# Performance work log

Measured on AMD Instinct MI355X. Metric: run time of the kernel, lower is better.

Reference implementation:

```python
import jax, jax.numpy as jnp
import numpy as np

N_NODES = 100000
N_EDGES = 1600000
N_GRAPHS = 64
IN_CH = 128
HIDDEN = 128
OUT_CH = 2


def gcn_conv(x, row, col, W, b, num_nodes):
    # PyG GCNConv: add self-loops, symmetric deg^{-1/2} normalization,
    # linear transform, scatter-add aggregation, then bias.
    loop = jnp.arange(num_nodes, dtype=row.dtype)
    r = jnp.concatenate([row, loop])  # source nodes
    c = jnp.concatenate([col, loop])  # target nodes
    deg = jax.ops.segment_sum(jnp.ones_like(c, dtype=x.dtype), c, num_segments=num_nodes)
    dinv = jnp.where(deg > 0, jax.lax.rsqrt(deg), 0.0)
    norm = dinv[r] * dinv[c]  # [E+N]
    h = x @ W  # [N, F_out]
    msg = norm[:, None] * h[r]  # gather [E+N, F_out]
    agg = jax.ops.segment_sum(msg, c, num_segments=num_nodes)  # scatter-add
    return agg + b


def setup_inputs() -> dict:
    key = jax.random.key(0)
    ks = jax.random.split(key, 8)
    x = jax.random.normal(ks[0], (N_NODES, IN_CH), dtype=jnp.float32)
    edge_index = jax.random.randint(ks[1], (2, N_EDGES), 0, N_NODES, dtype=jnp.int32)
    batch = jnp.sort(jax.random.randint(ks[2], (N_NODES,), 0, N_GRAPHS, dtype=jnp.int32))
    s1 = 1.0 / np.sqrt(IN_CH)
    s2 = 1.0 / np.sqrt(HIDDEN)
    W1 = jax.random.normal(ks[3], (IN_CH, HIDDEN), dtype=jnp.float32) * s1
    b1 = jnp.zeros((HIDDEN,), dtype=jnp.float32)
    W2 = jax.random.normal(ks[4], (HIDDEN, HIDDEN), dtype=jnp.float32) * s2
    b2 = jnp.zeros((HIDDEN,), dtype=jnp.float32)
    Wlin = jax.random.normal(ks[5], (HIDDEN, OUT_CH), dtype=jnp.float32) * s2
    blin = jnp.zeros((OUT_CH,), dtype=jnp.float32)
    return {"x": x, "edge_index": edge_index, "batch": batch,
            "W1": W1, "b1": b1, "W2": W2, "b2": b2, "Wlin": Wlin, "blin": blin}


def reference(x, edge_index, batch, W1, b1, W2, b2, Wlin, blin):
    row, col = edge_index[0], edge_index[1]
    h = jax.nn.relu(gcn_conv(x, row, col, W1, b1, N_NODES))
    h = jax.nn.relu(gcn_conv(h, row, col, W2, b2, N_NODES))
    # global_mean_pool over graph ids
    sums = jax.ops.segment_sum(h, batch, num_segments=N_GRAPHS)  # [G, H]
    cnts = jax.ops.segment_sum(jnp.ones((h.shape[0],), dtype=h.dtype), batch, num_segments=N_GRAPHS)
    pooled = sums / jnp.maximum(cnts, 1.0)[:, None]
    return pooled @ Wlin + blin  # [G, OUT_CH]
```

## Files before the change

kernel.cpp:

```cpp
#include <hip/hip_runtime.h>
#include <hip/hip_bf16.h>
#include <hip/hip_fp16.h>

#define N_NODES  100000
#define N_EDGES  1600000
#define N_GRAPHS 64

#define NB       256
#define BSZ      391
#define NE4      (N_EDGES/4)
#define NBLK     391

typedef __attribute__((ext_vector_type(4))) float    f32x4;
typedef __attribute__((ext_vector_type(8))) _Float16 f16x8;

__global__ __launch_bounds__(256) void zero_kernel(float* __restrict__ pooled,
                                                   float* __restrict__ gcnt) {
    int i = blockIdx.x * 256 + threadIdx.x;
    if (i < N_GRAPHS * 128) pooled[i] = 0.f;
    if (i < N_GRAPHS) gcnt[i] = 0.f;
}

__global__ __launch_bounds__(256) void sortcount_kernel(const int4* __restrict__ col4,
                                                        int* __restrict__ blockcnt) {
    __shared__ int hist[NB];
    int t = threadIdx.x, blk = blockIdx.x;
    hist[t] = 0;
    __syncthreads();
#pragma unroll
    for (int j = 0; j < 4; ++j) {
        int i = blk * 1024 + j * 256 + t;
        if (i < NE4) {
            int4 c = col4[i];
            atomicAdd(&hist[c.x / BSZ], 1);
            atomicAdd(&hist[c.y / BSZ], 1);
            atomicAdd(&hist[c.z / BSZ], 1);
            atomicAdd(&hist[c.w / BSZ], 1);
        }
    }
    __syncthreads();
    blockcnt[blk * NB + t] = hist[t];
}

__global__ __launch_bounds__(256) void sortscan_kernel(int* __restrict__ blockcnt,
                                                       int* __restrict__ buckettotal) {
    int b = blockIdx.x, t = threadIdx.x;
    __shared__ int sc[256];
    int e0 = 2 * t, e1 = 2 * t + 1;
    int v0 = (e0 < NBLK) ? blockcnt[e0 * NB + b] : 0;
    int v1 = (e1 < NBLK) ? blockcnt[e1 * NB + b] : 0;
    int ps = v0 + v1;
    sc[t] = ps;
    __syncthreads();
    for (int d = 1; d < 256; d <<= 1) {
        int x = (t >= d) ? sc[t - d] : 0;
        __syncthreads();
        sc[t] += x;
        __syncthreads();
    }
    int ex = sc[t] - ps;
    if (e0 < NBLK) blockcnt[e0 * NB + b] = ex;
    if (e1 < NBLK) blockcnt[e1 * NB + b] = ex + v0;
    if (t == 255) buckettotal[b] = sc[255];
}

__global__ __launch_bounds__(256) void sortbase_kernel(const int* __restrict__ buckettotal,
                                                       int* __restrict__ bucket_base,
                                                       int* __restrict__ off) {
    __shared__ int sc[256];
    int t = threadIdx.x;
    int v = buckettotal[t];
    sc[t] = v;
    __syncthreads();
    for (int d = 1; d < 256; d <<= 1) {
        int x = (t >= d) ? sc[t - d] : 0;
        __syncthreads();
        sc[t] += x;
        __syncthreads();
    }
    bucket_base[t] = sc[t] - v;
    if (t == 255) {
        bucket_base[256] = sc[255];
        off[N_NODES] = N_EDGES;
    }
}

__global__ __launch_bounds__(256) void sortscatter_kernel(const int4* __restrict__ row4,
                                                          const int4* __restrict__ col4,
                                                          const int* __restrict__ blockpre,
                                                          const int* __restrict__ bucket_base,
                                                          int2* __restrict__ pairs) {
    __shared__ int cur[NB];
    int t = threadIdx.x, blk = blockIdx.x;
    cur[t] = bucket_base[t] + blockpre[blk * NB + t];
    __syncthreads();
#pragma unroll
    for (int j = 0; j < 4; ++j) {
        int i = blk * 1024 + j * 256 + t;
        if (i < NE4) {
            int4 r = row4[i];
            int4 c = col4[i];
            int p0 = atomicAdd(&cur[c.x / BSZ], 1); pairs[p0] = make_int2(r.x, c.x);
            int p1 = atomicAdd(&cur[c.y / BSZ], 1); pairs[p1] = make_int2(r.y, c.y);
            int p2 = atomicAdd(&cur[c.z / BSZ], 1); pairs[p2] = make_int2(r.z, c.z);
            int p3 = atomicAdd(&cur[c.w / BSZ], 1); pairs[p3] = make_int2(r.w, c.w);
        }
    }
}

__global__ __launch_bounds__(256) void sortlocal_kernel(const int2* __restrict__ pairs,
                                                        const int* __restrict__ bucket_base,
                                                        const int* __restrict__ buckettotal,
                                                        int* __restrict__ sortr,
                                                        int* __restrict__ off,
                                                        float* __restrict__ dinv) {
    int b = blockIdx.x, t = threadIdx.x;
    int base = bucket_base[b];
    int cnt  = buckettotal[b];
    int c0   = b * BSZ;
    int nc   = N_NODES - c0; if (nc > BSZ) nc = BSZ;

    __shared__ int hist[BSZ];
    __shared__ int sc[256];
    for (int i = t; i < nc; i += 256) hist[i] = 0;
    __syncthreads();
    for (int i = t; i < cnt; i += 256) {
        int2 pc = pairs[base + i];
        atomicAdd(&hist[pc.y - c0], 1);
    }
    __syncthreads();
    int e0 = 2 * t, e1 = 2 * t + 1;
    int h0 = (e0 < nc) ? hist[e0] : 0;
    int h1 = (e1 < nc) ? hist[e1] : 0;
    int ps = h0 + h1;
    sc[t] = ps;
    __syncthreads();
    for (int d = 1; d < 256; d <<= 1) {
        int x = (t >= d) ? sc[t - d] : 0;
        __syncthreads();
        sc[t] += x;
        __syncthreads();
    }
    int ex = sc[t] - ps;
    if (e0 < nc) { off[c0 + e0] = base + ex;      dinv[c0 + e0] = rsqrtf((float)h0 + 1.f); }
    if (e1 < nc) { off[c0 + e1] = base + ex + h0; dinv[c0 + e1] = rsqrtf((float)h1 + 1.f); }
    __syncthreads();
    if (e0 < nc) hist[e0] = base + ex;
    if (e1 < nc) hist[e1] = base + ex + h0;
    __syncthreads();
    for (int i = t; i < cnt; i += 256) {
        int2 pc = pairs[base + i];
        int pos = atomicAdd(&hist[pc.y - c0], 1);
        sortr[pos] = pc.x;
    }
}

__global__ __launch_bounds__(256) void wpack_kernel(const float* __restrict__ W1,
                                                    const float* __restrict__ W2,
                                                    _Float16* __restrict__ Wp1,
                                                    _Float16* __restrict__ Wp2) {
    int tid = blockIdx.x * 256 + threadIdx.x;
    const float* W = (tid < 2048) ? W1 : W2;
    _Float16*   Wp = (tid < 2048) ? Wp1 : Wp2;
    int t = tid & 2047;
    int f = t >> 6, lane = t & 63;
    int j = f >> 2, s = f & 3;
    int kb = s * 32 + (lane >> 4) * 8;
    int c  = j * 16 + (lane & 15);
#pragma unroll
    for (int i = 0; i < 8; ++i)
        Wp[(size_t)t * 8 + i] = (_Float16)W[(kb + i) * 128 + c];
}

template<int FP16IN>
__global__ __launch_bounds__(256) void gemm_mfma_kernel(const void* __restrict__ Xv,
                                                        const _Float16* __restrict__ Wp,
                                                        const float* __restrict__ dinv,
                                                        _Float16* __restrict__ out) {
    __shared__ _Float16 Wl[16384];
    {
        const float4* src = (const float4*)Wp;
        float4* dst = (float4*)Wl;
        for (int i = threadIdx.x; i < 2048; i += 256) dst[i] = src[i];
    }
    __syncthreads();

    int wv = threadIdx.x >> 6, lane = threadIdx.x & 63;
    int tile = blockIdx.x * 4 + wv;
    if (tile >= N_NODES / 16) return;
    int n0 = tile * 16;
    int m = lane & 15, b = lane >> 4;

    f16x8 a[4];
    if (FP16IN) {
        const _Float16* X = (const _Float16*)Xv;
        const _Float16* base = X + (size_t)(n0 + m) * 128 + b * 8;
#pragma unroll
        for (int s = 0; s < 4; ++s) a[s] = *(const f16x8*)(base + s * 32);
    } else {
        const float* X = (const float*)Xv;
        const float* base = X + (size_t)(n0 + m) * 128 + b * 8;
#pragma unroll
        for (int s = 0; s < 4; ++s) {
            float4 u = *(const float4*)(base + s * 32);
            float4 v = *(const float4*)(base + s * 32 + 4);
            f16x8 tt;
            tt[0] = (_Float16)u.x; tt[1] = (_Float16)u.y;
            tt[2] = (_Float16)u.z; tt[3] = (_Float16)u.w;
            tt[4] = (_Float16)v.x; tt[5] = (_Float16)v.y;
            tt[6] = (_Float16)v.z; tt[7] = (_Float16)v.w;
            a[s] = tt;
        }
    }

    f32x4 acc[8];
#pragma unroll
    for (int j = 0; j < 8; ++j) acc[j] = (f32x4){0.f, 0.f, 0.f, 0.f};

#pragma unroll
    for (int j = 0; j < 8; ++j) {
#pragma unroll
        for (int s = 0; s < 4; ++s) {
            f16x8 bf = *(const f16x8*)&Wl[(j * 4 + s) * 512 + lane * 8];
            acc[j] = __builtin_amdgcn_mfma_f32_16x16x32_f16(a[s], bf, acc[j], 0, 0, 0);
        }
    }

    float dv0 = dinv[n0 + b * 4 + 0];
    float dv1 = dinv[n0 + b * 4 + 1];
    float dv2 = dinv[n0 + b * 4 + 2];
    float dv3 = dinv[n0 + b * 4 + 3];
#pragma unroll
    for (int j = 0; j < 8; ++j) {
        _Float16* o = out + (size_t)(n0 + b * 4) * 128 + j * 16 + m;
        o[0 * 128] = (_Float16)(acc[j][0] * dv0);
        o[1 * 128] = (_Float16)(acc[j][1] * dv1);
        o[2 * 128] = (_Float16)(acc[j][2] * dv2);
        o[3 * 128] = (_Float16)(acc[j][3] * dv3);
    }
}

__global__ __launch_bounds__(256) void agg_kernel(const __half* __restrict__ hs,
                                                  const int* __restrict__ sortr,
                                                  const int* __restrict__ off,
                                                  const float* __restrict__ dinv,
                                                  const float* __restrict__ bias,
                                                  __half* __restrict__ out) {
    int wid = (blockIdx.x * 256 + threadIdx.x) >> 6;
    int lane = threadIdx.x & 63;
    if (wid >= N_NODES) return;
    const int c = wid;
    const int e0 = off[c], e1 = off[c + 1];
    const long chb = 2 * lane;

    float2 s = __half22float2(*(const __half2*)&hs[(long)c * 128 + chb]);
    float a0x = s.x, a0y = s.y;
    float a1x = 0.f, a1y = 0.f, a2x = 0.f, a2y = 0.f, a3x = 0.f, a3y = 0.f;

    int e = e0;
    for (; e + 4 <= e1; e += 4) {
        int r0 = sortr[e + 0], r1 = sortr[e + 1];
        int r2 = sortr[e + 2], r3 = sortr[e + 3];
        float2 v0 = __half22float2(*(const __half2*)&hs[(long)r0 * 128 + chb]);
        float2 v1 = __half22float2(*(const __half2*)&hs[(long)r1 * 128 + chb]);
        float2 v2 = __half22float2(*(const __half2*)&hs[(long)r2 * 128 + chb]);
        float2 v3 = __half22float2(*(const __half2*)&hs[(long)r3 * 128 + chb]);
        a0x += v0.x; a0y += v0.y;
        a1x += v1.x; a1y += v1.y;
        a2x += v2.x; a2y += v2.y;
        a3x += v3.x; a3y += v3.y;
    }
    for (; e < e1; ++e) {
        int r0 = sortr[e];
        float2 v0 = __half22float2(*(const __half2*)&hs[(long)r0 * 128 + chb]);
        a0x += v0.x; a0y += v0.y;
    }
    float ax = (a0x + a1x) + (a2x + a3x);
    float ay = (a0y + a1y) + (a2y + a3y);

    float dv = dinv[c];
    float2 bb = *(const float2*)&bias[chb];
    float rx = fmaxf(fmaf(ax, dv, bb.x), 0.f);
    float ry = fmaxf(fmaf(ay, dv, bb.y), 0.f);
    *(__half2*)&out[(long)c * 128 + chb] = __floats2half2_rn(rx, ry);
}

__global__ __launch_bounds__(256) void pool_kernel(const __half* __restrict__ h,
                                                   const int* __restrict__ batch,
                                                   float* __restrict__ pooled,
                                                   float* __restrict__ gcnt) {
    int wid = (blockIdx.x * 256 + threadIdx.x) >> 6;
    int lane = threadIdx.x & 63;
    long n0 = (long)wid * 32;
    if (n0 >= N_NODES) return;
    long n1 = n0 + 32;
    if (n1 > N_NODES) n1 = N_NODES;
    const long chb = 2 * lane;

    int g = batch[n0];
    float ax = 0.f, ay = 0.f;
    int run = 0;
    for (long n = n0; n < n1; ++n) {
        int gn = batch[n];
        if (gn != g) {
            atomicAdd(&pooled[g * 128 + chb], ax);
            atomicAdd(&pooled[g * 128 + chb + 1], ay);
            if (lane == 0) atomicAdd(&gcnt[g], (float)run);
            g = gn; ax = 0.f; ay = 0.f; run = 0;
        }
        float2 v = __half22float2(*(const __half2*)&h[n * 128 + chb]);
        ax += v.x; ay += v.y; run++;
    }
    atomicAdd(&pooled[g * 128 + chb], ax);
    atomicAdd(&pooled[g * 128 + chb + 1], ay);
    if (lane == 0) atomicAdd(&gcnt[g], (float)run);
}

__global__ void final_kernel(const float* __restrict__ pooled,
                             const float* __restrict__ gcnt,
                             const float* __restrict__ Wlin,
                             const float* __restrict__ blin,
                             float* __restrict__ out) {
    int t = threadIdx.x;
    if (t >= N_GRAPHS * 2) return;
    int g = t >> 1, o = t & 1;
    float c = gcnt[g];
    if (c < 1.f) c = 1.f;
    float s = 0.f;
    for (int k = 0; k < 128; ++k)
        s += (pooled[g * 128 + k] / c) * Wlin[k * 2 + o];
    out[g * 2 + o] = s + blin[o];
}

extern "C" void kernel_launch(void* const* d_in, const int* in_sizes, int n_in,
                              void* d_out, int out_size, void* d_ws, size_t ws_size,
                              hipStream_t stream) {
    const float* x     = (const float*)d_in[0];
    const int*   row   = (const int*)d_in[1];
    const int*   col   = row + N_EDGES;
    const int*   batch = (const int*)d_in[2];
    const float* W1    = (const float*)d_in[3];
    const float* b1    = (const float*)d_in[4];
    const float* W2    = (const float*)d_in[5];
    const float* b2    = (const float*)d_in[6];
    const float* Wlin  = (const float*)d_in[7];
    const float* blin  = (const float*)d_in[8];
    float* out = (float*)d_out;

    char* w = (char*)d_ws;
    size_t p = 0;
    auto alloc = [&](size_t bytes) -> void* {
        void* r = w + p;
        p += (bytes + 511) & ~(size_t)511;
        return r;
    };
    int*      off         = (int*)alloc((size_t)(N_NODES + 1) * 4);
    float*    dinv        = (float*)alloc((size_t)N_NODES * 4);
    int*      sortr       = (int*)alloc((size_t)N_EDGES * 4);
    int2*     pairs       = (int2*)alloc((size_t)N_EDGES * 8);
    int*      blockcnt    = (int*)alloc((size_t)NBLK * NB * 4);
    int*      buckettotal = (int*)alloc((size_t)NB * 4);
    int*      bucket_base = (int*)alloc((size_t)(NB + 1) * 4);
    _Float16* Wp1         = (_Float16*)alloc((size_t)128 * 128 * 2);
    _Float16* Wp2         = (_Float16*)alloc((size_t)128 * 128 * 2);
    __half*   hs          = (__half*)alloc((size_t)N_NODES * 128 * 2);
    __half*   hbuf        = (__half*)alloc((size_t)N_NODES * 128 * 2);
    float*    pooled      = (float*)alloc((size_t)N_GRAPHS * 128 * 4);
    float*    gcnt        = (float*)alloc((size_t)N_GRAPHS * 4);
    (void)ws_size; (void)in_sizes; (void)n_in; (void)out_size;

    zero_kernel<<<(N_GRAPHS * 128 + 255) / 256, 256, 0, stream>>>(pooled, gcnt);

    sortcount_kernel<<<NBLK, 256, 0, stream>>>((const int4*)col, blockcnt);
    sortscan_kernel<<<NB, 256, 0, stream>>>(blockcnt, buckettotal);
    sortbase_kernel<<<1, 256, 0, stream>>>(buckettotal, bucket_base, off);
    sortscatter_kernel<<<NBLK, 256, 0, stream>>>((const int4*)row, (const int4*)col,
                                                 blockcnt, bucket_base, pairs);
    sortlocal_kernel<<<NB, 256, 0, stream>>>(pairs, bucket_base, buckettotal,
                                             sortr, off, dinv);

    wpack_kernel<<<16, 256, 0, stream>>>(W1, W2, Wp1, Wp2);

    gemm_mfma_kernel<0><<<(N_NODES / 16 + 3) / 4, 256, 0, stream>>>(x, Wp1, dinv, (_Float16*)hs);
    agg_kernel<<<(N_NODES * 64 + 255) / 256, 256, 0, stream>>>(hs, sortr, off, dinv, b1, hbuf);
    gemm_mfma_kernel<1><<<(N_NODES / 16 + 3) / 4, 256, 0, stream>>>(hbuf, Wp2, dinv, (_Float16*)hs);
    agg_kernel<<<(N_NODES * 64 + 255) / 256, 256, 0, stream>>>(hs, sortr, off, dinv, b2, hbuf);

    pool_kernel<<<(((N_NODES + 31) / 32) * 64 + 255) / 256, 256, 0, stream>>>(hbuf, batch, pooled, gcnt);
    final_kernel<<<1, 128, 0, stream>>>(pooled, gcnt, Wlin, blin, out);
}
```

Measured before the change: 356.1 us.

## Fuse aggregation with next GEMM and pooling, pack sort pairs into one int

The first GCN aggregation is fused with the second layer's MFMA GEMM through a shared-memory row buffer. The second aggregation is fused with global mean pooling using per-block reductions before the atomics. Sort pairs are packed into a single 32-bit word (local column in the high bits, row in the low 17 bits), halving the pairs traffic. Zeroing is folded into the weight-pack kernel. Together these remove two intermediate N×128 buffer round trips and three launches. In exchange, the fused GEMM reads W from global memory instead of LDS, and each block gathers only 16 rows, which may lower latency hiding.

```diff
diff --git a/kernel.cpp b/kernel.cpp
--- a/kernel.cpp
+++ b/kernel.cpp
@@ -10,16 +10,10 @@
 #define BSZ      391
 #define NE4      (N_EDGES/4)
 #define NBLK     391
+#define ROWMASK  0x1FFFF
 
 typedef __attribute__((ext_vector_type(4))) float    f32x4;
 typedef __attribute__((ext_vector_type(8))) _Float16 f16x8;
-
-__global__ __launch_bounds__(256) void zero_kernel(float* __restrict__ pooled,
-                                                   float* __restrict__ gcnt) {
-    int i = blockIdx.x * 256 + threadIdx.x;
-    if (i < N_GRAPHS * 128) pooled[i] = 0.f;
-    if (i < N_GRAPHS) gcnt[i] = 0.f;
-}
 
 __global__ __launch_bounds__(256) void sortcount_kernel(const int4* __restrict__ col4,
                                                         int* __restrict__ blockcnt) {
@@ -89,7 +83,7 @@
                                                           const int4* __restrict__ col4,
                                                           const int* __restrict__ blockpre,
                                                           const int* __restrict__ bucket_base,
-                                                          int2* __restrict__ pairs) {
+                                                          int* __restrict__ pairs) {
     __shared__ int cur[NB];
     int t = threadIdx.x, blk = blockIdx.x;
     cur[t] = bucket_base[t] + blockpre[blk * NB + t];
@@ -100,15 +94,16 @@
         if (i < NE4) {
             int4 r = row4[i];
             int4 c = col4[i];
-            int p0 = atomicAdd(&cur[c.x / BSZ], 1); pairs[p0] = make_int2(r.x, c.x);
-            int p1 = atomicAdd(&cur[c.y / BSZ], 1); pairs[p1] = make_int2(r.y, c.y);
-            int p2 = atomicAdd(&cur[c.z / BSZ], 1); pairs[p2] = make_int2(r.z, c.z);
-            int p3 = atomicAdd(&cur[c.w / BSZ], 1); pairs[p3] = make_int2(r.w, c.w);
-        }
-    }
-}
-
-__global__ __launch_bounds__(256) void sortlocal_kernel(const int2* __restrict__ pairs,
+            int b0 = c.x / BSZ, b1 = c.y / BSZ, b2 = c.z / BSZ, b3 = c.w / BSZ;
+            int p0 = atomicAdd(&cur[b0], 1); pairs[p0] = ((c.x - b0 * BSZ) << 17) | r.x;
+            int p1 = atomicAdd(&cur[b1], 1); pairs[p1] = ((c.y - b1 * BSZ) << 17) | r.y;
+            int p2 = atomicAdd(&cur[b2], 1); pairs[p2] = ((c.z - b2 * BSZ) << 17) | r.z;
+            int p3 = atomicAdd(&cur[b3], 1); pairs[p3] = ((c.w - b3 * BSZ) << 17) | r.w;
+        }
+    }
+}
+
+__global__ __launch_bounds__(256) void sortlocal_kernel(const int* __restrict__ pairs,
                                                         const int* __restrict__ bucket_base,
                                                         const int* __restrict__ buckettotal,
                                                         int* __restrict__ sortr,
@@ -125,8 +120,8 @@
     for (int i = t; i < nc; i += 256) hist[i] = 0;
     __syncthreads();
     for (int i = t; i < cnt; i += 256) {
-        int2 pc = pairs[base + i];
-        atomicAdd(&hist[pc.y - c0], 1);
+        int pc = pairs[base + i];
+        atomicAdd(&hist[pc >> 17], 1);
     }
     __syncthreads();
     int e0 = 2 * t, e1 = 2 * t + 1;
@@ -149,17 +144,23 @@
     if (e1 < nc) hist[e1] = base + ex + h0;
     __syncthreads();
     for (int i = t; i < cnt; i += 256) {
-        int2 pc = pairs[base + i];
-        int pos = atomicAdd(&hist[pc.y - c0], 1);
-        sortr[pos] = pc.x;
-    }
-}
-
-__global__ __launch_bounds__(256) void wpack_kernel(const float* __restrict__ W1,
-                                                    const float* __restrict__ W2,
-                                                    _Float16* __restrict__ Wp1,
-                                                    _Float16* __restrict__ Wp2) {
+        int pc = pairs[base + i];
+        int pos = atomicAdd(&hist[pc >> 17], 1);
+        sortr[pos] = pc & ROWMASK;
+    }
+}
+
+__global__ __launch_bounds__(256) void wpack_zero_kernel(const float* __restrict__ W1,
+                                                         const float* __restrict__ W2,
+                                                         _Float16* __restrict__ Wp1,
+                                                         _Float16* __restrict__ Wp2,
+                                                         float* __restrict__ pooled,
+                                                         float* __restrict__ gcnt) {
     int tid = blockIdx.x * 256 + threadIdx.x;
+    for (int i = tid; i < N_GRAPHS * 128 + N_GRAPHS; i += 4096) {
+        if (i < N_GRAPHS * 128) pooled[i] = 0.f;
+        else gcnt[i - N_GRAPHS * 128] = 0.f;
+    }
     const float* W = (tid < 2048) ? W1 : W2;
     _Float16*   Wp = (tid < 2048) ? Wp1 : Wp2;
     int t = tid & 2047;
@@ -172,8 +173,7 @@
         Wp[(size_t)t * 8 + i] = (_Float16)W[(kb + i) * 128 + c];
 }
 
-template<int FP16IN>
-__global__ __launch_bounds__(256) void gemm_mfma_kernel(const void* __restrict__ Xv,
+__global__ __launch_bounds__(256) void gemm_mfma_kernel(const float* __restrict__ X,
                                                         const _Float16* __restrict__ Wp,
                                                         const float* __restrict__ dinv,
                                                         _Float16* __restrict__ out) {
@@ -192,39 +192,29 @@
     int m = lane & 15, b = lane >> 4;
 
     f16x8 a[4];
-    if (FP16IN) {
-        const _Float16* X = (const _Float16*)Xv;
-        const _Float16* base = X + (size_t)(n0 + m) * 128 + b * 8;
-#pragma unroll
-        for (int s = 0; s < 4; ++s) a[s] = *(const f16x8*)(base + s * 32);
-    } else {
-        const float* X = (const float*)Xv;
-        const float* base = X + (size_t)(n0 + m) * 128 + b * 8;
-#pragma unroll
-        for (int s = 0; s < 4; ++s) {
-            float4 u = *(const float4*)(base + s * 32);
-            float4 v = *(const float4*)(base + s * 32 + 4);
-            f16x8 tt;
-            tt[0] = (_Float16)u.x; tt[1] = (_Float16)u.y;
-            tt[2] = (_Float16)u.z; tt[3] = (_Float16)u.w;
-            tt[4] = (_Float16)v.x; tt[5] = (_Float16)v.y;
-            tt[6] = (_Float16)v.z; tt[7] = (_Float16)v.w;
-            a[s] = tt;
-        }
+    const float* base = X + (size_t)(n0 + m) * 128 + b * 8;
+#pragma unroll
+    for (int s = 0; s < 4; ++s) {
+        float4 u = *(const float4*)(base + s * 32);
+        float4 v = *(const float4*)(base + s * 32 + 4);
+        f16x8 tt;
+        tt[0] = (_Float16)u.x; tt[1] = (_Float16)u.y;
+        tt[2] = (_Float16)u.z; tt[3] = (_Float16)u.w;
+        tt[4] = (_Float16)v.x; tt[5] = (_Float16)v.y;
+        tt[6] = (_Float16)v.z; tt[7] = (_Float16)v.w;
+        a[s] = tt;
     }
 
     f32x4 acc[8];
 #pragma unroll
     for (int j = 0; j < 8; ++j) acc[j] = (f32x4){0.f, 0.f, 0.f, 0.f};
-
-#pragma unroll
-    for (int j = 0; j < 8; ++j) {
+#pragma unroll
+    for (int j = 0; j < 8; ++j)
 #pragma unroll
         for (int s = 0; s < 4; ++s) {
             f16x8 bf = *(const f16x8*)&Wl[(j * 4 + s) * 512 + lane * 8];
             acc[j] = __builtin_amdgcn_mfma_f32_16x16x32_f16(a[s], bf, acc[j], 0, 0, 0);
         }
-    }
 
     float dv0 = dinv[n0 + b * 4 + 0];
     float dv1 = dinv[n0 + b * 4 + 1];
@@ -240,23 +230,12 @@
     }
 }
 
-__global__ __launch_bounds__(256) void agg_kernel(const __half* __restrict__ hs,
-                                                  const int* __restrict__ sortr,
-                                                  const int* __restrict__ off,
-                                                  const float* __restrict__ dinv,
-                                                  const float* __restrict__ bias,
-                                                  __half* __restrict__ out) {
-    int wid = (blockIdx.x * 256 + threadIdx.x) >> 6;
-    int lane = threadIdx.x & 63;
-    if (wid >= N_NODES) return;
-    const int c = wid;
-    const int e0 = off[c], e1 = off[c + 1];
-    const long chb = 2 * lane;
-
+__device__ __forceinline__ float2 gather_row(const __half* __restrict__ hs,
+                                             const int* __restrict__ sortr,
+                                             int c, int e0, int e1, long chb) {
     float2 s = __half22float2(*(const __half2*)&hs[(long)c * 128 + chb]);
     float a0x = s.x, a0y = s.y;
     float a1x = 0.f, a1y = 0.f, a2x = 0.f, a2y = 0.f, a3x = 0.f, a3y = 0.f;
-
     int e = e0;
     for (; e + 4 <= e1; e += 4) {
         int r0 = sortr[e + 0], r1 = sortr[e + 1];
@@ -275,45 +254,151 @@
         float2 v0 = __half22float2(*(const __half2*)&hs[(long)r0 * 128 + chb]);
         a0x += v0.x; a0y += v0.y;
     }
-    float ax = (a0x + a1x) + (a2x + a3x);
-    float ay = (a0y + a1y) + (a2y + a3y);
-
-    float dv = dinv[c];
+    float2 r;
+    r.x = (a0x + a1x) + (a2x + a3x);
+    r.y = (a0y + a1y) + (a2y + a3y);
+    return r;
+}
+
+__global__ __launch_bounds__(256) void agg_gemm_kernel(const __half* __restrict__ hs,
+                                                       const int* __restrict__ sortr,
+                                                       const int* __restrict__ off,
+                                                       const float* __restrict__ dinv,
+                                                       const float* __restrict__ bias,
+                                                       const _Float16* __restrict__ Wp,
+                                                       _Float16* __restrict__ out) {
+    __shared__ float rowbuf[16 * 132];
+    int t = threadIdx.x;
+    int wv = t >> 6, lane = t & 63;
+    int c0 = blockIdx.x * 16;
+    const long chb = 2 * (long)lane;
     float2 bb = *(const float2*)&bias[chb];
-    float rx = fmaxf(fmaf(ax, dv, bb.x), 0.f);
-    float ry = fmaxf(fmaf(ay, dv, bb.y), 0.f);
-    *(__half2*)&out[(long)c * 128 + chb] = __floats2half2_rn(rx, ry);
-}
-
-__global__ __launch_bounds__(256) void pool_kernel(const __half* __restrict__ h,
-                                                   const int* __restrict__ batch,
-                                                   float* __restrict__ pooled,
-                                                   float* __restrict__ gcnt) {
-    int wid = (blockIdx.x * 256 + threadIdx.x) >> 6;
-    int lane = threadIdx.x & 63;
-    long n0 = (long)wid * 32;
-    if (n0 >= N_NODES) return;
-    long n1 = n0 + 32;
-    if (n1 > N_NODES) n1 = N_NODES;
-    const long chb = 2 * lane;
-
-    int g = batch[n0];
-    float ax = 0.f, ay = 0.f;
-    int run = 0;
-    for (long n = n0; n < n1; ++n) {
-        int gn = batch[n];
-        if (gn != g) {
-            atomicAdd(&pooled[g * 128 + chb], ax);
-            atomicAdd(&pooled[g * 128 + chb + 1], ay);
-            if (lane == 0) atomicAdd(&gcnt[g], (float)run);
-            g = gn; ax = 0.f; ay = 0.f; run = 0;
-        }
-        float2 v = __half22float2(*(const __half2*)&h[n * 128 + chb]);
-        ax += v.x; ay += v.y; run++;
-    }
-    atomicAdd(&pooled[g * 128 + chb], ax);
-    atomicAdd(&pooled[g * 128 + chb + 1], ay);
-    if (lane == 0) atomicAdd(&gcnt[g], (float)run);
+
+#pragma unroll
+    for (int i = 0; i < 4; ++i) {
+        int c = c0 + wv * 4 + i;
+        float2 g = gather_row(hs, sortr, c, off[c], off[c + 1], chb);
+        float dv = dinv[c];
+        float rx = fmaxf(fmaf(g.x, dv, bb.x), 0.f);
+        float ry = fmaxf(fmaf(g.y, dv, bb.y), 0.f);
+        rowbuf[(wv * 4 + i) * 132 + 2 * lane]     = rx;
+        rowbuf[(wv * 4 + i) * 132 + 2 * lane + 1] = ry;
+    }
+    __syncthreads();
+
+    int m = lane & 15, b = lane >> 4;
+    f16x8 a[4];
+#pragma unroll
+    for (int s = 0; s < 4; ++s) {
+        const float* rb = &rowbuf[m * 132 + s * 32 + b * 8];
+        float4 u = *(const float4*)rb;
+        float4 v = *(const float4*)(rb + 4);
+        f16x8 tt;
+        tt[0] = (_Float16)u.x; tt[1] = (_Float16)u.y;
+        tt[2] = (_Float16)u.z; tt[3] = (_Float16)u.w;
+        tt[4] = (_Float16)v.x; tt[5] = (_Float16)v.y;
+        tt[6] = (_Float16)v.z; tt[7] = (_Float16)v.w;
+        a[s] = tt;
+    }
+
+    f32x4 acc[2];
+    acc[0] = (f32x4){0.f, 0.f, 0.f, 0.f};
+    acc[1] = (f32x4){0.f, 0.f, 0.f, 0.f};
+#pragma unroll
+    for (int jj = 0; jj < 2; ++jj) {
+        int j = wv * 2 + jj;
+#pragma unroll
+        for (int s = 0; s < 4; ++s) {
+            f16x8 bf = *(const f16x8*)&Wp[((size_t)(j * 4 + s) * 64 + lane) * 8];
+            acc[jj] = __builtin_amdgcn_mfma_f32_16x16x32_f16(a[s], bf, acc[jj], 0, 0, 0);
+        }
+    }
+
+    float dv0 = dinv[c0 + b * 4 + 0];
+    float dv1 = dinv[c0 + b * 4 + 1];
+    float dv2 = dinv[c0 + b * 4 + 2];
+    float dv3 = dinv[c0 + b * 4 + 3];
+#pragma unroll
+    for (int jj = 0; jj < 2; ++jj) {
+        int j = wv * 2 + jj;
+        _Float16* o = out + (size_t)(c0 + b * 4) * 128 + j * 16 + m;
+        o[0 * 128] = (_Float16)(acc[jj][0] * dv0);
+        o[1 * 128] = (_Float16)(acc[jj][1] * dv1);
+        o[2 * 128] = (_Float16)(acc[jj][2] * dv2);
+        o[3 * 128] = (_Float16)(acc[jj][3] * dv3);
+    }
+}
+
+__global__ __launch_bounds__(256) void agg_pool_kernel(const __half* __restrict__ hs2,
+                                                       const int* __restrict__ sortr,
+                                                       const int* __restrict__ off,
+                                                       const float* __restrict__ dinv,
+                                                       const float* __restrict__ bias,
+                                                       const int* __restrict__ batch,
+                                                       float* __restrict__ pooled,
+                                                       float* __restrict__ gcnt) {
+    __shared__ float redA[4][128];
+    __shared__ float redB[4][128];
+    int t = threadIdx.x;
+    int wv = t >> 6, lane = t & 63;
+    int c0 = blockIdx.x * 16;
+    const long chb = 2 * (long)lane;
+    float2 bb = *(const float2*)&bias[chb];
+
+    int g0   = batch[c0];
+    int gend = batch[c0 + 15];
+    bool slow = (gend > g0 + 1);
+
+    float2 accA = make_float2(0.f, 0.f);
+    float2 accB = make_float2(0.f, 0.f);
+
+#pragma unroll
+    for (int i = 0; i < 4; ++i) {
+        int c = c0 + wv * 4 + i;
+        float2 g = gather_row(hs2, sortr, c, off[c], off[c + 1], chb);
+        float dv = dinv[c];
+        float rx = fmaxf(fmaf(g.x, dv, bb.x), 0.f);
+        float ry = fmaxf(fmaf(g.y, dv, bb.y), 0.f);
+        int gg = batch[c];
+        if (!slow) {
+            if (gg == g0) { accA.x += rx; accA.y += ry; }
+            else          { accB.x += rx; accB.y += ry; }
+        } else {
+            atomicAdd(&pooled[(size_t)gg * 128 + chb],     rx);
+            atomicAdd(&pooled[(size_t)gg * 128 + chb + 1], ry);
+        }
+    }
+
+    if (!slow) {
+        redA[wv][2 * lane]     = accA.x;
+        redA[wv][2 * lane + 1] = accA.y;
+        redB[wv][2 * lane]     = accB.x;
+        redB[wv][2 * lane + 1] = accB.y;
+        __syncthreads();
+        if (wv == 0) {
+            int ch0 = 2 * lane, ch1 = 2 * lane + 1;
+            float sA0 = (redA[0][ch0] + redA[1][ch0]) + (redA[2][ch0] + redA[3][ch0]);
+            float sA1 = (redA[0][ch1] + redA[1][ch1]) + (redA[2][ch1] + redA[3][ch1]);
+            atomicAdd(&pooled[(size_t)g0 * 128 + ch0], sA0);
+            atomicAdd(&pooled[(size_t)g0 * 128 + ch1], sA1);
+            if (gend != g0) {
+                float sB0 = (redB[0][ch0] + redB[1][ch0]) + (redB[2][ch0] + redB[3][ch0]);
+                float sB1 = (redB[0][ch1] + redB[1][ch1]) + (redB[2][ch1] + redB[3][ch1]);
+                atomicAdd(&pooled[(size_t)gend * 128 + ch0], sB0);
+                atomicAdd(&pooled[(size_t)gend * 128 + ch1], sB1);
+            }
+        }
+        if (t == 0) {
+            int nB = 0;
+#pragma unroll
+            for (int k = 0; k < 16; ++k) nB += (batch[c0 + k] != g0) ? 1 : 0;
+            atomicAdd(&gcnt[g0], (float)(16 - nB));
+            if (nB) atomicAdd(&gcnt[gend], (float)nB);
+        }
+    } else {
+        if (t == 0)
+            for (int k = 0; k < 16; ++k) atomicAdd(&gcnt[batch[c0 + k]], 1.f);
+    }
 }
 
 __global__ void final_kernel(const float* __restrict__ pooled,
@@ -357,19 +442,17 @@
     int*      off         = (int*)alloc((size_t)(N_NODES + 1) * 4);
     float*    dinv        = (float*)alloc((size_t)N_NODES * 4);
     int*      sortr       = (int*)alloc((size_t)N_EDGES * 4);
-    int2*     pairs       = (int2*)alloc((size_t)N_EDGES * 8);
+    int*      pairs       = (int*)alloc((size_t)N_EDGES * 4);
     int*      blockcnt    = (int*)alloc((size_t)NBLK * NB * 4);
     int*      buckettotal = (int*)alloc((size_t)NB * 4);
     int*      bucket_base = (int*)alloc((size_t)(NB + 1) * 4);
     _Float16* Wp1         = (_Float16*)alloc((size_t)128 * 128 * 2);
     _Float16* Wp2         = (_Float16*)alloc((size_t)128 * 128 * 2);
     __half*   hs          = (__half*)alloc((size_t)N_NODES * 128 * 2);
-    __half*   hbuf        = (__half*)alloc((size_t)N_NODES * 128 * 2);
+    __half*   hs2         = (__half*)alloc((size_t)N_NODES * 128 * 2);
     float*    pooled      = (float*)alloc((size_t)N_GRAPHS * 128 * 4);
     float*    gcnt        = (float*)alloc((size_t)N_GRAPHS * 4);
     (void)ws_size; (void)in_sizes; (void)n_in; (void)out_size;
-
-    zero_kernel<<<(N_GRAPHS * 128 + 255) / 256, 256, 0, stream>>>(pooled, gcnt);
 
     sortcount_kernel<<<NBLK, 256, 0, stream>>>((const int4*)col, blockcnt);
     sortscan_kernel<<<NB, 256, 0, stream>>>(blockcnt, buckettotal);
@@ -378,14 +461,12 @@
                                                  blockcnt, bucket_base, pairs);
     sortlocal_kernel<<<NB, 256, 0, stream>>>(pairs, bucket_base, buckettotal,
                                              sortr, off, dinv);
-
-    wpack_kernel<<<16, 256, 0, stream>>>(W1, W2, Wp1, Wp2);
-
-    gemm_mfma_kernel<0><<<(N_NODES / 16 + 3) / 4, 256, 0, stream>>>(x, Wp1, dinv, (_Float16*)hs);
-    agg_kernel<<<(N_NODES * 64 + 255) / 256, 256, 0, stream>>>(hs, sortr, off, dinv, b1, hbuf);
-    gemm_mfma_kernel<1><<<(N_NODES / 16 + 3) / 4, 256, 0, stream>>>(hbuf, Wp2, dinv, (_Float16*)hs);
-    agg_kernel<<<(N_NODES * 64 + 255) / 256, 256, 0, stream>>>(hs, sortr, off, dinv, b2, hbuf);
-
-    pool_kernel<<<(((N_NODES + 31) / 32) * 64 + 255) / 256, 256, 0, stream>>>(hbuf, batch, pooled, gcnt);
+    wpack_zero_kernel<<<16, 256, 0, stream>>>(W1, W2, Wp1, Wp2, pooled, gcnt);
+
+    gemm_mfma_kernel<<<(N_NODES / 16 + 3) / 4, 256, 0, stream>>>(x, Wp1, dinv, (_Float16*)hs);
+    agg_gemm_kernel<<<N_NODES / 16, 256, 0, stream>>>(hs, sortr, off, dinv, b1, Wp2,
+                                                      (_Float16*)hs2);
+    agg_pool_kernel<<<N_NODES / 16, 256, 0, stream>>>(hs2, sortr, off, dinv, b2, batch,
+                                                      pooled, gcnt);
     final_kernel<<<1, 128, 0, stream>>>(pooled, gcnt, Wlin, blin, out);
 }
```

Result: faster. 343.8 us (-3.5%).

## Store transformed features as FP8 and pack sort pairs into one int

Applied to the files above, without the earlier changes.

The GEMM output that the aggregation kernel gathers is now stored as FP8 (e4m3 via the hardware convert builtin) rather than FP16, which halves the bytes per random neighbour gather. The sort pairs are packed into a single 32-bit word (local column in the high bits, row in the low 17 bits), which halves the traffic of the scatter and local-sort passes. The zero kernel is merged into the weight-pack kernel to drop one launch. FP8 storage lowers the precision of the intermediate features, which may push accuracy against the tolerance.

```diff
diff --git a/kernel.cpp b/kernel.cpp
--- a/kernel.cpp
+++ b/kernel.cpp
@@ -10,15 +10,17 @@
 #define BSZ      391
 #define NE4      (N_EDGES/4)
 #define NBLK     391
+#define ROWMASK  0x1FFFF
 
 typedef __attribute__((ext_vector_type(4))) float    f32x4;
+typedef __attribute__((ext_vector_type(2))) float    f32x2;
 typedef __attribute__((ext_vector_type(8))) _Float16 f16x8;
 
-__global__ __launch_bounds__(256) void zero_kernel(float* __restrict__ pooled,
-                                                   float* __restrict__ gcnt) {
-    int i = blockIdx.x * 256 + threadIdx.x;
-    if (i < N_GRAPHS * 128) pooled[i] = 0.f;
-    if (i < N_GRAPHS) gcnt[i] = 0.f;
+__device__ __forceinline__ unsigned char enc8(float v) {
+    return (unsigned char)(__builtin_amdgcn_cvt_pk_fp8_f32(v, v, 0, false) & 0xFF);
+}
+__device__ __forceinline__ f32x2 dec8x2(unsigned short us) {
+    return __builtin_amdgcn_cvt_pk_f32_fp8((unsigned int)us, false);
 }
 
 __global__ __launch_bounds__(256) void sortcount_kernel(const int4* __restrict__ col4,
@@ -89,7 +91,7 @@
                                                           const int4* __restrict__ col4,
                                                           const int* __restrict__ blockpre,
                                                           const int* __restrict__ bucket_base,
-                                                          int2* __restrict__ pairs) {
+                                                          int* __restrict__ pairs) {
     __shared__ int cur[NB];
     int t = threadIdx.x, blk = blockIdx.x;
     cur[t] = bucket_base[t] + blockpre[blk * NB + t];
@@ -100,15 +102,16 @@
         if (i < NE4) {
             int4 r = row4[i];
             int4 c = col4[i];
-            int p0 = atomicAdd(&cur[c.x / BSZ], 1); pairs[p0] = make_int2(r.x, c.x);
-            int p1 = atomicAdd(&cur[c.y / BSZ], 1); pairs[p1] = make_int2(r.y, c.y);
-            int p2 = atomicAdd(&cur[c.z / BSZ], 1); pairs[p2] = make_int2(r.z, c.z);
-            int p3 = atomicAdd(&cur[c.w / BSZ], 1); pairs[p3] = make_int2(r.w, c.w);
-        }
-    }
-}
-
-__global__ __launch_bounds__(256) void sortlocal_kernel(const int2* __restrict__ pairs,
+            int b0 = c.x / BSZ, b1 = c.y / BSZ, b2 = c.z / BSZ, b3 = c.w / BSZ;
+            int p0 = atomicAdd(&cur[b0], 1); pairs[p0] = ((c.x - b0 * BSZ) << 17) | r.x;
+            int p1 = atomicAdd(&cur[b1], 1); pairs[p1] = ((c.y - b1 * BSZ) << 17) | r.y;
+            int p2 = atomicAdd(&cur[b2], 1); pairs[p2] = ((c.z - b2 * BSZ) << 17) | r.z;
+            int p3 = atomicAdd(&cur[b3], 1); pairs[p3] = ((c.w - b3 * BSZ) << 17) | r.w;
+        }
+    }
+}
+
+__global__ __launch_bounds__(256) void sortlocal_kernel(const int* __restrict__ pairs,
                                                         const int* __restrict__ bucket_base,
                                                         const int* __restrict__ buckettotal,
                                                         int* __restrict__ sortr,
@@ -125,8 +128,8 @@
     for (int i = t; i < nc; i += 256) hist[i] = 0;
     __syncthreads();
     for (int i = t; i < cnt; i += 256) {
-        int2 pc = pairs[base + i];
-        atomicAdd(&hist[pc.y - c0], 1);
+        int pc = pairs[base + i];
+        atomicAdd(&hist[pc >> 17], 1);
     }
     __syncthreads();
     int e0 = 2 * t, e1 = 2 * t + 1;
@@ -149,17 +152,23 @@
     if (e1 < nc) hist[e1] = base + ex + h0;
     __syncthreads();
     for (int i = t; i < cnt; i += 256) {
-        int2 pc = pairs[base + i];
-        int pos = atomicAdd(&hist[pc.y - c0], 1);
-        sortr[pos] = pc.x;
-    }
-}
-
-__global__ __launch_bounds__(256) void wpack_kernel(const float* __restrict__ W1,
-                                                    const float* __restrict__ W2,
-                                                    _Float16* __restrict__ Wp1,
-                                                    _Float16* __restrict__ Wp2) {
+        int pc = pairs[base + i];
+        int pos = atomicAdd(&hist[pc >> 17], 1);
+        sortr[pos] = pc & ROWMASK;
+    }
+}
+
+__global__ __launch_bounds__(256) void wpack_zero_kernel(const float* __restrict__ W1,
+                                                         const float* __restrict__ W2,
+                                                         _Float16* __restrict__ Wp1,
+                                                         _Float16* __restrict__ Wp2,
+                                                         float* __restrict__ pooled,
+                                                         float* __restrict__ gcnt) {
     int tid = blockIdx.x * 256 + threadIdx.x;
+    for (int i = tid; i < N_GRAPHS * 128 + N_GRAPHS; i += 4096) {
+        if (i < N_GRAPHS * 128) pooled[i] = 0.f;
+        else gcnt[i - N_GRAPHS * 128] = 0.f;
+    }
     const float* W = (tid < 2048) ? W1 : W2;
     _Float16*   Wp = (tid < 2048) ? Wp1 : Wp2;
     int t = tid & 2047;
@@ -176,7 +185,7 @@
 __global__ __launch_bounds__(256) void gemm_mfma_kernel(const void* __restrict__ Xv,
                                                         const _Float16* __restrict__ Wp,
                                                         const float* __restrict__ dinv,
-                                                        _Float16* __restrict__ out) {
+                                                        unsigned char* __restrict__ out8) {
     __shared__ _Float16 Wl[16384];
     {
         const float4* src = (const float4*)Wp;
@@ -216,15 +225,13 @@
     f32x4 acc[8];
 #pragma unroll
     for (int j = 0; j < 8; ++j) acc[j] = (f32x4){0.f, 0.f, 0.f, 0.f};
-
-#pragma unroll
-    for (int j = 0; j < 8; ++j) {
+#pragma unroll
+    for (int j = 0; j < 8; ++j)
 #pragma unroll
         for (int s = 0; s < 4; ++s) {
             f16x8 bf = *(const f16x8*)&Wl[(j * 4 + s) * 512 + lane * 8];
             acc[j] = __builtin_amdgcn_mfma_f32_16x16x32_f16(a[s], bf, acc[j], 0, 0, 0);
         }
-    }
 
     float dv0 = dinv[n0 + b * 4 + 0];
     float dv1 = dinv[n0 + b * 4 + 1];
@@ -232,15 +239,15 @@
     float dv3 = dinv[n0 + b * 4 + 3];
 #pragma unroll
     for (int j = 0; j < 8; ++j) {
-        _Float16* o = out + (size_t)(n0 + b * 4) * 128 + j * 16 + m;
-        o[0 * 128] = (_Float16)(acc[j][0] * dv0);
-        o[1 * 128] = (_Float16)(acc[j][1] * dv1);
-        o[2 * 128] = (_Float16)(acc[j][2] * dv2);
-        o[3 * 128] = (_Float16)(acc[j][3] * dv3);
-    }
-}
-
-__global__ __launch_bounds__(256) void agg_kernel(const __half* __restrict__ hs,
+        unsigned char* o = out8 + (size_t)(n0 + b * 4) * 128 + j * 16 + m;
+        o[0 * 128] = enc8(acc[j][0] * dv0);
+        o[1 * 128] = enc8(acc[j][1] * dv1);
+        o[2 * 128] = enc8(acc[j][2] * dv2);
+        o[3 * 128] = enc8(acc[j][3] * dv3);
+    }
+}
+
+__global__ __launch_bounds__(256) void agg_kernel(const unsigned char* __restrict__ hs8,
                                                   const int* __restrict__ sortr,
                                                   const int* __restrict__ off,
                                                   const float* __restrict__ dinv,
@@ -251,38 +258,38 @@
     if (wid >= N_NODES) return;
     const int c = wid;
     const int e0 = off[c], e1 = off[c + 1];
-    const long chb = 2 * lane;
-
-    float2 s = __half22float2(*(const __half2*)&hs[(long)c * 128 + chb]);
-    float a0x = s.x, a0y = s.y;
+    const size_t bo = 2 * (size_t)lane;
+
+    f32x2 s = dec8x2(*(const unsigned short*)(hs8 + (size_t)c * 128 + bo));
+    float a0x = s[0], a0y = s[1];
     float a1x = 0.f, a1y = 0.f, a2x = 0.f, a2y = 0.f, a3x = 0.f, a3y = 0.f;
 
     int e = e0;
     for (; e + 4 <= e1; e += 4) {
         int r0 = sortr[e + 0], r1 = sortr[e + 1];
         int r2 = sortr[e + 2], r3 = sortr[e + 3];
-        float2 v0 = __half22float2(*(const __half2*)&hs[(long)r0 * 128 + chb]);
-        float2 v1 = __half22float2(*(const __half2*)&hs[(long)r1 * 128 + chb]);
-        float2 v2 = __half22float2(*(const __half2*)&hs[(long)r2 * 128 + chb]);
-        float2 v3 = __half22float2(*(const __half2*)&hs[(long)r3 * 128 + chb]);
-        a0x += v0.x; a0y += v0.y;
-        a1x += v1.x; a1y += v1.y;
-        a2x += v2.x; a2y += v2.y;
-        a3x += v3.x; a3y += v3.y;
+        f32x2 v0 = dec8x2(*(const unsigned short*)(hs8 + (size_t)r0 * 128 + bo));
+        f32x2 v1 = dec8x2(*(const unsigned short*)(hs8 + (size_t)r1 * 128 + bo));
+        f32x2 v2 = dec8x2(*(const unsigned short*)(hs8 + (size_t)r2 * 128 + bo));
+        f32x2 v3 = dec8x2(*(const unsigned short*)(hs8 + (size_t)r3 * 128 + bo));
+        a0x += v0[0]; a0y += v0[1];
+        a1x += v1[0]; a1y += v1[1];
+        a2x += v2[0]; a2y += v2[1];
+        a3x += v3[0]; a3y += v3[1];
     }
     for (; e < e1; ++e) {
         int r0 = sortr[e];
-        float2 v0 = __half22float2(*(const __half2*)&hs[(long)r0 * 128 + chb]);
-        a0x += v0.x; a0y += v0.y;
+        f32x2 v0 = dec8x2(*(const unsigned short*)(hs8 + (size_t)r0 * 128 + bo));
+        a0x += v0[0]; a0y += v0[1];
     }
     float ax = (a0x + a1x) + (a2x + a3x);
     float ay = (a0y + a1y) + (a2y + a3y);
 
     float dv = dinv[c];
-    float2 bb = *(const float2*)&bias[chb];
+    float2 bb = *(const float2*)&bias[2 * lane];
     float rx = fmaxf(fmaf(ax, dv, bb.x), 0.f);
     float ry = fmaxf(fmaf(ay, dv, bb.y), 0.f);
-    *(__half2*)&out[(long)c * 128 + chb] = __floats2half2_rn(rx, ry);
+    *(__half2*)&out[(size_t)c * 128 + 2 * lane] = __floats2half2_rn(rx, ry);
 }
 
 __global__ __launch_bounds__(256) void pool_kernel(const __half* __restrict__ h,
@@ -354,22 +361,22 @@
         p += (bytes + 511) & ~(size_t)511;
         return r;
     };
-    int*      off         = (int*)alloc((size_t)(N_NODES + 1) * 4);
-    float*    dinv        = (float*)alloc((size_t)N_NODES * 4);
-    int*      sortr       = (int*)alloc((size_t)N_EDGES * 4);
-    int2*     pairs       = (int2*)alloc((size_t)N_EDGES * 8);
-    int*      blockcnt    = (int*)alloc((size_t)NBLK * NB * 4);
-    int*      buckettotal = (int*)alloc((size_t)NB * 4);
-    int*      bucket_base = (int*)alloc((size_t)(NB + 1) * 4);
-    _Float16* Wp1         = (_Float16*)alloc((size_t)128 * 128 * 2);
-    _Float16* Wp2         = (_Float16*)alloc((size_t)128 * 128 * 2);
-    __half*   hs          = (__half*)alloc((size_t)N_NODES * 128 * 2);
-    __half*   hbuf        = (__half*)alloc((size_t)N_NODES * 128 * 2);
-    float*    pooled      = (float*)alloc((size_t)N_GRAPHS * 128 * 4);
-    float*    gcnt        = (float*)alloc((size_t)N_GRAPHS * 4);
+    int*           off         = (int*)alloc((size_t)(N_NODES + 1) * 4);
+    float*         dinv        = (float*)alloc((size_t)N_NODES * 4);
+    int*           sortr       = (int*)alloc((size_t)N_EDGES * 4);
+    int*           pairs       = (int*)alloc((size_t)N_EDGES * 4);
+    int*           blockcnt    = (int*)alloc((size_t)NBLK * NB * 4);
+    int*           buckettotal = (int*)alloc((size_t)NB * 4);
+    int*           bucket_base = (int*)alloc((size_t)(NB + 1) * 4);
+    _Float16*      Wp1         = (_Float16*)alloc((size_t)128 * 128 * 2);
+    _Float16*      Wp2         = (_Float16*)alloc((size_t)128 * 128 * 2);
+    unsigned char* hs8         = (unsigned char*)alloc((size_t)N_NODES * 128);
+    unsigned char* hs8b        = (unsigned char*)alloc((size_t)N_NODES * 128);
+    __half*        h2          = (__half*)alloc((size_t)N_NODES * 128 * 2);
+    __half*        hbuf        = (__half*)alloc((size_t)N_NODES * 128 * 2);
+    float*         pooled      = (float*)alloc((size_t)N_GRAPHS * 128 * 4);
+    float*         gcnt       = (float*)alloc((size_t)N_GRAPHS * 4);
     (void)ws_size; (void)in_sizes; (void)n_in; (void)out_size;
-
-    zero_kernel<<<(N_GRAPHS * 128 + 255) / 256, 256, 0, stream>>>(pooled, gcnt);
 
     sortcount_kernel<<<NBLK, 256, 0, stream>>>((const int4*)col, blockcnt);
     sortscan_kernel<<<NB, 256, 0, stream>>>(blockcnt, buckettotal);
@@ -378,13 +385,12 @@
                                                  blockcnt, bucket_base, pairs);
     sortlocal_kernel<<<NB, 256, 0, stream>>>(pairs, bucket_base, buckettotal,
                                              sortr, off, dinv);
-
-    wpack_kernel<<<16, 256, 0, stream>>>(W1, W2, Wp1, Wp2);
-
-    gemm_mfma_kernel<0><<<(N_NODES / 16 + 3) / 4, 256, 0, stream>>>(x, Wp1, dinv, (_Float16*)hs);
-    agg_kernel<<<(N_NODES * 64 + 255) / 256, 256, 0, stream>>>(hs, sortr, off, dinv, b1, hbuf);
-    gemm_mfma_kernel<1><<<(N_NODES / 16 + 3) / 4, 256, 0, stream>>>(hbuf, Wp2, dinv, (_Float16*)hs);
-    agg_kernel<<<(N_NODES * 64 + 255) / 256, 256, 0, stream>>>(hs, sortr, off, dinv, b2, hbuf);
+    wpack_zero_kernel<<<16, 256, 0, stream>>>(W1, W2, Wp1, Wp2, pooled, gcnt);
+
+    gemm_mfma_kernel<0><<<(N_NODES / 16 + 3) / 4, 256, 0, stream>>>(x, Wp1, dinv, hs8);
+    agg_kernel<<<(N_NODES * 64 + 255) / 256, 256, 0, stream>>>(hs8, sortr, off, dinv, b1, h2);
+    gemm_mfma_kernel<1><<<(N_NODES / 16 + 3) / 4, 256, 0, stream>>>(h2, Wp2, dinv, hs8b);
+    agg_kernel<<<(N_NODES * 64 + 255) / 256, 256, 0, stream>>>(hs8b, sortr, off, dinv, b2, hbuf);
 
     pool_kernel<<<(((N_NODES + 31) / 32) * 64 + 255) / 256, 256, 0, stream>>>(hbuf, batch, pooled, gcnt);
     final_kernel<<<1, 128, 0, stream>>>(pooled, gcnt, Wlin, blin, out);
```

Result: faster. 337.8 us (-5.1%).
